# Performance work log

Measured on AMD Instinct MI355X. Metric: run time of the kernel, lower is better.

## Reference

```python
import jax, jax.numpy as jnp
import numpy as np

# Config mirrors cfg['cluster'] and point_cloud_range from init_kwargs
PCR = np.array([-51.2, -51.2, -5.0, 51.2, 51.2, 3.0], dtype=np.float32)
VOXEL_SIZE = 0.2
SIZE_X = 512  # floor((51.2 - (-51.2)) / 0.2)
EPS = 1.5
MIN_SAMPLES = 5
MIN_P_CLUSTER = 20


def _cluster(points):
    """Faithful jax version of Cluster.forward for batch_size == 1.

    voxel_down_sample -> DBSCAN (euclidean, eps, min_samples) on voxel coords
    -> drop clusters with < MIN_P_CLUSTER voxels -> scatter labels back to points.
    """
    N = points.shape[0]
    # --- voxel_down_sample ---
    coords = jnp.floor((points[:, 1:3] - PCR[:2]) / VOXEL_SIZE).astype(jnp.int32)  # (N,2) x,y
    merged = coords[:, 1] * SIZE_X + coords[:, 0]
    # static-size unique: padded entries get fill_value=-1 at the end
    uniq, inv = jnp.unique(merged, size=N, fill_value=-1, return_inverse=True)
    valid = uniq >= 0  # (N,) real voxels
    vox = jnp.stack([uniq % SIZE_X, uniq // SIZE_X], axis=1).astype(jnp.float32)  # (N,2)

    # --- DBSCAN on voxel coords ---
    d2 = jnp.sum((vox[:, None, :] - vox[None, :, :]) ** 2, axis=-1)  # (N,N)
    adj = (d2 <= EPS * EPS) & valid[:, None] & valid[None, :]  # includes self-edge
    core = (jnp.sum(adj, axis=1) >= MIN_SAMPLES) & valid  # sklearn counts self

    BIG = N  # sentinel > any label
    labels0 = jnp.where(core, jnp.arange(N), BIG)
    adj_core = adj & core[None, :]

    def min_core_neighbor(labels):
        return jnp.min(jnp.where(adj_core, labels[None, :], BIG), axis=1)

    def body(carry):
        labels, _ = carry
        new = jnp.where(core, jnp.minimum(labels, min_core_neighbor(labels)), labels)
        return new, jnp.any(new != labels)

    # min-label propagation = connected components over core-core eps graph
    labels, _ = jax.lax.while_loop(lambda c: c[1], body, (labels0, jnp.array(True)))

    # border points attach to a neighboring core cluster; otherwise noise (-1)
    nb = min_core_neighbor(labels)
    raw = jnp.where(core, labels, jnp.where(valid & (nb < BIG), nb, -1))  # root-id or -1

    # relabel root-ids to consecutive 0..k-1 (sklearn numbering by smallest core idx)
    roots = jnp.unique(raw, size=N, fill_value=BIG)  # sorted; BIG padding at end
    pos = jnp.searchsorted(roots, raw)
    dense = pos - (roots[0] == -1).astype(pos.dtype)
    dense = jnp.where(raw >= 0, dense, -1)

    # drop small clusters (by voxel count), keep remaining ids unchanged
    counts = jnp.zeros(N, jnp.int32).at[jnp.where(dense >= 0, dense, 0)].add(
        jnp.where(dense >= 0, 1, 0))
    keep = counts >= MIN_P_CLUSTER
    final = jnp.where((dense >= 0) & keep[jnp.clip(dense, 0, N - 1)], dense, -1)

    # scatter voxel labels back to points (points_inst_idx has points.dtype, like torch)
    pts_inst = final[inv].astype(points.dtype)
    max_num_inst = jnp.maximum(jnp.max(final) + 1, 0)
    return pts_inst, max_num_inst


def setup_inputs() -> dict:
    key = jax.random.key(0)
    N = 8192
    k1, k2, k3, k4, k5, k6, k7 = jax.random.split(key, 7)
    n_blobs = 64
    centers = jax.random.uniform(k1, (n_blobs, 2), minval=-48.0, maxval=48.0)
    assign = jax.random.randint(k2, (N,), 0, n_blobs)
    xy = centers[assign] + jax.random.normal(k3, (N, 2)) * 1.0
    noise = jax.random.uniform(k4, (N,)) < 0.2
    xy = jnp.where(noise[:, None], jax.random.uniform(k5, (N, 2), minval=-51.0, maxval=51.0), xy)
    xy = jnp.clip(xy, -51.0, 51.0)
    z = jax.random.uniform(k6, (N, 1), minval=-3.0, maxval=1.0)
    feat = jax.random.normal(k7, (N, 1))
    points = jnp.concatenate([jnp.zeros((N, 1)), xy, z, feat], axis=1).astype(jnp.float32)
    return {"points": points, "batch_size": 1}


def reference(points, batch_size):
    # voxel_down_sample asserts batch_size == 1; single-batch path.
    return _cluster(points)
```

## Files before the change

kernel.cpp:

```cpp
#include <hip/hip_runtime.h>
#include <stdint.h>


#define GRIDW 512
#define WPR 16
#define NWORDS 8192
#define NCELLS 262144
#define NONE 0xFFFFFFFFu

#define OFF_OCC    0
#define OFF_CNT    8192
#define OFF_ROOTBM 16384
#define OFF_KEEPBM 16640
#define OFF_CM     16896
#define OFF_LAB    25088
#define OFF_PRE    33280
#define OFF_RPRE   41472

__device__ __forceinline__ void hsum(uint32_t l, uint32_t c, uint32_t r,
                                     uint32_t& h0, uint32_t& h1) {
  uint32_t Wb = (c << 1) | (l >> 31);
  uint32_t Eb = (c >> 1) | (r << 31);
  h0 = Wb ^ c ^ Eb;
  h1 = (Wb & c) | (Eb & (Wb ^ c));
}

__device__ __forceinline__ uint32_t ge5(uint32_t a0, uint32_t a1, uint32_t b0,
                                        uint32_t b1, uint32_t c0, uint32_t c1) {
  uint32_t u0 = a0 ^ b0, cy = a0 & b0;
  uint32_t t = a1 ^ b1;
  uint32_t u1 = t ^ cy;
  uint32_t u2 = (a1 & b1) | (cy & t);
  uint32_t v0 = u0 ^ c0, k0 = u0 & c0;
  uint32_t t2 = u1 ^ c1;
  uint32_t v1 = t2 ^ k0;
  uint32_t k1 = (u1 & c1) | (k0 & t2);
  uint32_t v2 = u2 ^ k1;
  uint32_t v3 = u2 & k1;
  return v3 | (v2 & (v1 | v0));
}

__device__ __forceinline__ uint32_t aread(uint32_t* p) {
  return __hip_atomic_load(p, __ATOMIC_RELAXED, __HIP_MEMORY_SCOPE_AGENT);
}

__device__ __forceinline__ uint32_t findc(uint32_t* L, uint32_t x) {
  uint32_t r = x, p = aread(&L[r]);
  while (p != r) { r = p; p = aread(&L[r]); }
  while (x > r) {
    uint32_t nx = aread(&L[x]);
    if (nx <= r) break;
    atomicCAS(&L[x], nx, r);
    x = nx;
  }
  return r;
}

__device__ __forceinline__ void unite(uint32_t* L, uint32_t a, uint32_t b) {
  for (;;) {
    a = findc(L, a);
    b = findc(L, b);
    if (a == b) return;
    uint32_t lo = min(a, b), hi = max(a, b);
    if (atomicCAS(&L[hi], hi, lo) == hi) return;
    a = lo; b = hi;
  }
}

__global__ void k_vox(const float* __restrict__ pts, uint32_t* __restrict__ ws,
                      int npts) {
  int i = blockIdx.x * 256 + threadIdx.x;
  if (i >= npts) return;
  float x = pts[i * 5 + 1];
  float y = pts[i * 5 + 2];
  int cx = (int)floorf((x - (-51.2f)) / 0.2f);
  int cy = (int)floorf((y - (-51.2f)) / 0.2f);
  cx = min(max(cx, 0), GRIDW - 1);
  cy = min(max(cy, 0), GRIDW - 1);
  int cell = cy * GRIDW + cx;
  atomicOr(&ws[OFF_OCC + (cell >> 5)], 1u << (cell & 31));
}

__global__ void k_scan_cm(uint32_t* __restrict__ ws) {
  const uint32_t* occ = ws + OFF_OCC;
  int tid = threadIdx.x;
  if (blockIdx.x == 0) {
    __shared__ uint32_t wsum[4];
    ws[OFF_ROOTBM + tid] = 0u;
    ws[OFF_KEEPBM + tid] = 0u;
    int base = tid * 32;
    uint32_t s = 0;
    for (int j = 0; j < 32; j++) s += __popc(occ[base + j]);
    int lane = tid & 63, wv = tid >> 6;
    uint32_t inc = s;
    for (int d = 1; d < 64; d <<= 1) { uint32_t t = __shfl_up(inc, d); if (lane >= d) inc += t; }
    if (lane == 63) wsum[wv] = inc;
    __syncthreads();
    uint32_t woff = 0;
    for (int k = 0; k < wv; k++) woff += wsum[k];
    uint32_t excl = woff + inc - s;
    uint32_t* pre = ws + OFF_PRE;
    for (int j = 0; j < 32; j++) { pre[base + j] = excl; excl += __popc(occ[base + j]); }
  } else {
    int wi = (blockIdx.x - 1) * 256 + tid;
    ws[OFF_LAB + wi] = (uint32_t)wi;
    ws[OFF_CNT + wi] = 0u;
    uint32_t cB = occ[wi];
    int y = wi >> 4, wx = wi & 15;
    uint32_t lB = wx ? occ[wi - 1] : 0u;
    uint32_t rB = (wx < 15) ? occ[wi + 1] : 0u;
    uint32_t cA = 0, lA = 0, rA = 0, cC = 0, lC = 0, rC = 0;
    if (y > 0) { int wa = wi - WPR; cA = occ[wa]; lA = wx ? occ[wa - 1] : 0u; rA = (wx < 15) ? occ[wa + 1] : 0u; }
    if (y < GRIDW - 1) { int wc = wi + WPR; cC = occ[wc]; lC = wx ? occ[wc - 1] : 0u; rC = (wx < 15) ? occ[wc + 1] : 0u; }
    uint32_t a0, a1, b0, b1, c0, c1;
    hsum(lA, cA, rA, a0, a1); hsum(lB, cB, rB, b0, b1); hsum(lC, cC, rC, c0, c1);
    ws[OFF_CM + wi] = ge5(a0, a1, b0, b1, c0, c1) & cB;
  }
}

__global__ void k_merge(uint32_t* __restrict__ ws) {
  int cell = blockIdx.x * 256 + threadIdx.x;
  const uint32_t* occ = ws + OFF_OCC;
  const uint32_t* cm = ws + OFF_CM;
  const uint32_t* pre = ws + OFF_PRE;
  uint32_t* lab = ws + OFF_LAB;
  int wi = cell >> 5, b = cell & 31, wx = wi & 15;
  uint32_t cw = cm[wi];
  if (!((cw >> b) & 1)) return;
  int y = cell >> 9;
  uint32_t cB = occ[wi];
  int r = pre[wi] + __popc(cB & ((1u << b) - 1u));
  bool eC = (b < 31) ? ((cw >> (b + 1)) & 1) : ((wx < 15) ? (cm[wi + 1] & 1) : false);
  if (eC) unite(lab, r, (b < 31) ? r + 1 : pre[wi + 1]);
  if (y < GRIDW - 1) {
    uint32_t cmS = cm[wi + WPR];
    uint32_t occS = occ[wi + WPR];
    int rS = pre[wi + WPR];
    if ((cmS >> b) & 1) unite(lab, r, rS + __popc(occS & ((1u << b) - 1u)));
    bool seC = (b < 31) ? ((cmS >> (b + 1)) & 1) : ((wx < 15) ? (cm[wi + WPR + 1] & 1) : false);
    if (seC) unite(lab, r, (b < 31) ? rS + __popc(occS & ((2u << b) - 1u)) : pre[wi + WPR + 1]);
    bool swC = (b > 0) ? ((cmS >> (b - 1)) & 1) : ((wx > 0) ? (cm[wi + WPR - 1] >> 31) : false);
    if (swC) unite(lab, r, (b > 0) ? rS + __popc(occS & ((1u << (b - 1)) - 1u)) : rS - 1);
  }
}

__global__ void k_cb(uint32_t* __restrict__ ws) {
  int cell = blockIdx.x * 256 + threadIdx.x;
  int wi = cell >> 5, b = cell & 31, wx = wi & 15;
  const uint32_t* occ = ws + OFF_OCC;
  uint32_t cB = occ[wi];
  if (!((cB >> b) & 1)) return;
  const uint32_t* cm = ws + OFF_CM;
  const uint32_t* pre = ws + OFF_PRE;
  uint32_t* lab = ws + OFF_LAB;
  uint32_t* cnt = ws + OFF_CNT;
  int y = cell >> 9;
  uint32_t cw = cm[wi];
  int r = pre[wi] + __popc(cB & ((1u << b) - 1u));
  if ((cw >> b) & 1) {
    uint32_t root = findc(lab, r);
    lab[r] = root;
    if (root == (uint32_t)r) atomicOr(&ws[OFF_ROOTBM + (r >> 5)], 1u << (r & 31));
    atomicAdd(&cnt[root], 1u);
  } else {
    uint32_t m = NONE;
    bool wC = (b > 0) ? ((cw >> (b - 1)) & 1) : ((wx > 0) ? (cm[wi - 1] >> 31) : false);
    if (wC) m = min(m, findc(lab, (b > 0) ? r - 1 : (int)pre[wi] - 1));
    bool eC = (b < 31) ? ((cw >> (b + 1)) & 1) : ((wx < 15) ? (cm[wi + 1] & 1) : false);
    if (eC) m = min(m, findc(lab, (b < 31) ? r + 1 : pre[wi + 1]));
    if (y > 0) {
      uint32_t cmN = cm[wi - WPR], occN = occ[wi - WPR];
      int rN = pre[wi - WPR];
      if ((cmN >> b) & 1) m = min(m, findc(lab, rN + __popc(occN & ((1u << b) - 1u))));
      bool neC = (b < 31) ? ((cmN >> (b + 1)) & 1) : ((wx < 15) ? (cm[wi - WPR + 1] & 1) : false);
      if (neC) m = min(m, findc(lab, (b < 31) ? rN + __popc(occN & ((2u << b) - 1u)) : pre[wi - WPR + 1]));
      bool nwC = (b > 0) ? ((cmN >> (b - 1)) & 1) : ((wx > 0) ? (cm[wi - WPR - 1] >> 31) : false);
      if (nwC) m = min(m, findc(lab, (b > 0) ? rN + __popc(occN & ((1u << (b - 1)) - 1u)) : rN - 1));
    }
    if (y < GRIDW - 1) {
      uint32_t cmS = cm[wi + WPR], occS = occ[wi + WPR];
      int rS = pre[wi + WPR];
      if ((cmS >> b) & 1) m = min(m, findc(lab, rS + __popc(occS & ((1u << b) - 1u))));
      bool seC = (b < 31) ? ((cmS >> (b + 1)) & 1) : ((wx < 15) ? (cm[wi + WPR + 1] & 1) : false);
      if (seC) m = min(m, findc(lab, (b < 31) ? rS + __popc(occS & ((2u << b) - 1u)) : pre[wi + WPR + 1]));
      bool swC = (b > 0) ? ((cmS >> (b - 1)) & 1) : ((wx > 0) ? (cm[wi + WPR - 1] >> 31) : false);
      if (swC) m = min(m, findc(lab, (b > 0) ? rS + __popc(occS & ((1u << (b - 1)) - 1u)) : rS - 1));
    }
    lab[r] = m;
    if (m != NONE) atomicAdd(&cnt[m], 1u);
  }
}

__global__ void k_finish(uint32_t* __restrict__ ws, float* __restrict__ out,
                         int npts) {
  int tid = threadIdx.x;
  __shared__ uint32_t wsum[4];
  __shared__ int smax;
  if (tid == 0) smax = -1;
  __syncthreads();
  uint32_t rb = ws[OFF_ROOTBM + tid];
  uint32_t v = __popc(rb);
  int lane = tid & 63, wv = tid >> 6;
  uint32_t inc = v;
  for (int d = 1; d < 64; d <<= 1) { uint32_t t = __shfl_up(inc, d); if (lane >= d) inc += t; }
  if (lane == 63) wsum[wv] = inc;
  __syncthreads();
  uint32_t woff = 0;
  for (int k = 0; k < wv; k++) woff += wsum[k];
  uint32_t excl = woff + inc - v;
  ws[OFF_RPRE + tid] = excl;
  uint32_t keep = 0;
  int mx = -1, d = (int)excl;
  while (rb) {
    int b = __ffs(rb) - 1; rb &= rb - 1;
    int r = tid * 32 + b;
    if (ws[OFF_CNT + r] >= 20u) { keep |= 1u << b; mx = d; }
    d++;
  }
  ws[OFF_KEEPBM + tid] = keep;
  if (mx >= 0) atomicMax(&smax, mx);
  __syncthreads();
  if (tid == 0) out[npts] = (float)(smax + 1);
}

__global__ void k_scatter(const float* __restrict__ pts,
                          const uint32_t* __restrict__ ws,
                          float* __restrict__ out, int npts) {
  int i = blockIdx.x * 256 + threadIdx.x;
  if (i >= npts) return;
  float x = pts[i * 5 + 1];
  float y = pts[i * 5 + 2];
  int cx = (int)floorf((x - (-51.2f)) / 0.2f);
  int cy = (int)floorf((y - (-51.2f)) / 0.2f);
  cx = min(max(cx, 0), GRIDW - 1);
  cy = min(max(cy, 0), GRIDW - 1);
  int cell = cy * GRIDW + cx;
  int wi = cell >> 5;
  int r = ws[OFF_PRE + wi] + __popc(ws[OFF_OCC + wi] & ((1u << (cell & 31)) - 1u));
  uint32_t l = ws[OFF_LAB + r];
  float o = -1.0f;
  if (l != NONE && ((ws[OFF_KEEPBM + (l >> 5)] >> (l & 31)) & 1)) {
    int dnum = ws[OFF_RPRE + (l >> 5)] +
               __popc(ws[OFF_ROOTBM + (l >> 5)] & ((1u << (l & 31)) - 1u));
    o = (float)dnum;
  }
  out[i] = o;
}

extern "C" void kernel_launch(void* const* d_in, const int* in_sizes, int n_in,
                              void* d_out, int out_size, void* d_ws, size_t ws_size,
                              hipStream_t stream) {
  const float* pts = (const float*)d_in[0];
  int npts = in_sizes[0] / 5;
  uint32_t* ws = (uint32_t*)d_ws;
  float* out = (float*)d_out;
  int pblocks = (npts + 255) / 256;
  hipMemsetAsync(d_ws, 0, NWORDS * 4, stream);
  k_vox<<<pblocks, 256, 0, stream>>>(pts, ws, npts);
  k_scan_cm<<<33, 256, 0, stream>>>(ws);
  k_merge<<<NCELLS / 256, 256, 0, stream>>>(ws);
  k_cb<<<NCELLS / 256, 256, 0, stream>>>(ws);
  k_finish<<<1, 256, 0, stream>>>(ws, out, npts);
  k_scatter<<<pblocks, 256, 0, stream>>>(pts, ws, out, npts);
}
```

Measured before the change: 96.53 us.

## Fuse all clustering stages into one cooperative kernel with grid syncs

Replaces the memset and six separate kernel launches with a single cooperative kernel of 256 blocks. Stages are separated by grid-wide barriers, and grid-stride loops cover the cell and point work. This removes per-launch overhead and the inter-kernel gaps for a small workload. The cost is six grid syncs and lower parallelism in the per-cell stages, since 256 blocks now loop over 262144 cells.

```diff
diff --git a/kernel.cpp b/kernel.cpp
--- a/kernel.cpp
+++ b/kernel.cpp
@@ -1,5 +1,8 @@
 #include <hip/hip_runtime.h>
+#include <hip/hip_cooperative_groups.h>
 #include <stdint.h>
+
+namespace cg = cooperative_groups;
 
 
 #define GRIDW 512
@@ -67,27 +70,39 @@
   }
 }
 
-__global__ void k_vox(const float* __restrict__ pts, uint32_t* __restrict__ ws,
-                      int npts) {
-  int i = blockIdx.x * 256 + threadIdx.x;
-  if (i >= npts) return;
-  float x = pts[i * 5 + 1];
-  float y = pts[i * 5 + 2];
-  int cx = (int)floorf((x - (-51.2f)) / 0.2f);
-  int cy = (int)floorf((y - (-51.2f)) / 0.2f);
-  cx = min(max(cx, 0), GRIDW - 1);
-  cy = min(max(cy, 0), GRIDW - 1);
-  int cell = cy * GRIDW + cx;
-  atomicOr(&ws[OFF_OCC + (cell >> 5)], 1u << (cell & 31));
-}
-
-__global__ void k_scan_cm(uint32_t* __restrict__ ws) {
+__global__ __launch_bounds__(256) void k_all(const float* __restrict__ pts,
+                                             uint32_t* __restrict__ ws,
+                                             float* __restrict__ out,
+                                             int npts) {
+  cg::grid_group grid = cg::this_grid();
+  const int tid = threadIdx.x;
+  const int gtid = blockIdx.x * 256 + tid;
+  const int T = gridDim.x * 256;
+  __shared__ uint32_t wsum[4];
+  __shared__ int smax;
+
+  for (int i = gtid; i < NWORDS; i += T) {
+    ws[OFF_OCC + i] = 0u;
+    ws[OFF_CNT + i] = 0u;
+    ws[OFF_LAB + i] = (uint32_t)i;
+  }
+  if (gtid < 256) { ws[OFF_ROOTBM + gtid] = 0u; ws[OFF_KEEPBM + gtid] = 0u; }
+  grid.sync();
+
+  for (int i = gtid; i < npts; i += T) {
+    float x = pts[i * 5 + 1];
+    float y = pts[i * 5 + 2];
+    int cx = (int)floorf((x - (-51.2f)) / 0.2f);
+    int cy = (int)floorf((y - (-51.2f)) / 0.2f);
+    cx = min(max(cx, 0), GRIDW - 1);
+    cy = min(max(cy, 0), GRIDW - 1);
+    int cell = cy * GRIDW + cx;
+    atomicOr(&ws[OFF_OCC + (cell >> 5)], 1u << (cell & 31));
+  }
+  grid.sync();
+
   const uint32_t* occ = ws + OFF_OCC;
-  int tid = threadIdx.x;
   if (blockIdx.x == 0) {
-    __shared__ uint32_t wsum[4];
-    ws[OFF_ROOTBM + tid] = 0u;
-    ws[OFF_KEEPBM + tid] = 0u;
     int base = tid * 32;
     uint32_t s = 0;
     for (int j = 0; j < 32; j++) s += __popc(occ[base + j]);
@@ -102,149 +117,138 @@
     uint32_t* pre = ws + OFF_PRE;
     for (int j = 0; j < 32; j++) { pre[base + j] = excl; excl += __popc(occ[base + j]); }
   } else {
-    int wi = (blockIdx.x - 1) * 256 + tid;
-    ws[OFF_LAB + wi] = (uint32_t)wi;
-    ws[OFF_CNT + wi] = 0u;
-    uint32_t cB = occ[wi];
-    int y = wi >> 4, wx = wi & 15;
-    uint32_t lB = wx ? occ[wi - 1] : 0u;
-    uint32_t rB = (wx < 15) ? occ[wi + 1] : 0u;
-    uint32_t cA = 0, lA = 0, rA = 0, cC = 0, lC = 0, rC = 0;
-    if (y > 0) { int wa = wi - WPR; cA = occ[wa]; lA = wx ? occ[wa - 1] : 0u; rA = (wx < 15) ? occ[wa + 1] : 0u; }
-    if (y < GRIDW - 1) { int wc = wi + WPR; cC = occ[wc]; lC = wx ? occ[wc - 1] : 0u; rC = (wx < 15) ? occ[wc + 1] : 0u; }
-    uint32_t a0, a1, b0, b1, c0, c1;
-    hsum(lA, cA, rA, a0, a1); hsum(lB, cB, rB, b0, b1); hsum(lC, cC, rC, c0, c1);
-    ws[OFF_CM + wi] = ge5(a0, a1, b0, b1, c0, c1) & cB;
-  }
-}
-
-__global__ void k_merge(uint32_t* __restrict__ ws) {
-  int cell = blockIdx.x * 256 + threadIdx.x;
-  const uint32_t* occ = ws + OFF_OCC;
+    int wi = gtid - 256;
+    if (wi < NWORDS) {
+      uint32_t cB = occ[wi];
+      int y = wi >> 4, wx = wi & 15;
+      uint32_t lB = wx ? occ[wi - 1] : 0u;
+      uint32_t rB = (wx < 15) ? occ[wi + 1] : 0u;
+      uint32_t cA = 0, lA = 0, rA = 0, cC = 0, lC = 0, rC = 0;
+      if (y > 0) { int wa = wi - WPR; cA = occ[wa]; lA = wx ? occ[wa - 1] : 0u; rA = (wx < 15) ? occ[wa + 1] : 0u; }
+      if (y < GRIDW - 1) { int wc = wi + WPR; cC = occ[wc]; lC = wx ? occ[wc - 1] : 0u; rC = (wx < 15) ? occ[wc + 1] : 0u; }
+      uint32_t a0, a1, b0, b1, c0, c1;
+      hsum(lA, cA, rA, a0, a1); hsum(lB, cB, rB, b0, b1); hsum(lC, cC, rC, c0, c1);
+      ws[OFF_CM + wi] = ge5(a0, a1, b0, b1, c0, c1) & cB;
+    }
+  }
+  grid.sync();
+
   const uint32_t* cm = ws + OFF_CM;
   const uint32_t* pre = ws + OFF_PRE;
   uint32_t* lab = ws + OFF_LAB;
-  int wi = cell >> 5, b = cell & 31, wx = wi & 15;
-  uint32_t cw = cm[wi];
-  if (!((cw >> b) & 1)) return;
-  int y = cell >> 9;
-  uint32_t cB = occ[wi];
-  int r = pre[wi] + __popc(cB & ((1u << b) - 1u));
-  bool eC = (b < 31) ? ((cw >> (b + 1)) & 1) : ((wx < 15) ? (cm[wi + 1] & 1) : false);
-  if (eC) unite(lab, r, (b < 31) ? r + 1 : pre[wi + 1]);
-  if (y < GRIDW - 1) {
-    uint32_t cmS = cm[wi + WPR];
-    uint32_t occS = occ[wi + WPR];
-    int rS = pre[wi + WPR];
-    if ((cmS >> b) & 1) unite(lab, r, rS + __popc(occS & ((1u << b) - 1u)));
-    bool seC = (b < 31) ? ((cmS >> (b + 1)) & 1) : ((wx < 15) ? (cm[wi + WPR + 1] & 1) : false);
-    if (seC) unite(lab, r, (b < 31) ? rS + __popc(occS & ((2u << b) - 1u)) : pre[wi + WPR + 1]);
-    bool swC = (b > 0) ? ((cmS >> (b - 1)) & 1) : ((wx > 0) ? (cm[wi + WPR - 1] >> 31) : false);
-    if (swC) unite(lab, r, (b > 0) ? rS + __popc(occS & ((1u << (b - 1)) - 1u)) : rS - 1);
-  }
-}
-
-__global__ void k_cb(uint32_t* __restrict__ ws) {
-  int cell = blockIdx.x * 256 + threadIdx.x;
-  int wi = cell >> 5, b = cell & 31, wx = wi & 15;
-  const uint32_t* occ = ws + OFF_OCC;
-  uint32_t cB = occ[wi];
-  if (!((cB >> b) & 1)) return;
-  const uint32_t* cm = ws + OFF_CM;
-  const uint32_t* pre = ws + OFF_PRE;
-  uint32_t* lab = ws + OFF_LAB;
+  for (int cell = gtid; cell < NCELLS; cell += T) {
+    int wi = cell >> 5, b = cell & 31, wx = wi & 15;
+    uint32_t cw = cm[wi];
+    if (!((cw >> b) & 1)) continue;
+    int y = cell >> 9;
+    uint32_t cB = occ[wi];
+    int r = pre[wi] + __popc(cB & ((1u << b) - 1u));
+    bool eC = (b < 31) ? ((cw >> (b + 1)) & 1) : ((wx < 15) ? (cm[wi + 1] & 1) : false);
+    if (eC) unite(lab, r, (b < 31) ? r + 1 : pre[wi + 1]);
+    if (y < GRIDW - 1) {
+      uint32_t cmS = cm[wi + WPR];
+      uint32_t occS = occ[wi + WPR];
+      int rS = pre[wi + WPR];
+      if ((cmS >> b) & 1) unite(lab, r, rS + __popc(occS & ((1u << b) - 1u)));
+      bool seC = (b < 31) ? ((cmS >> (b + 1)) & 1) : ((wx < 15) ? (cm[wi + WPR + 1] & 1) : false);
+      if (seC) unite(lab, r, (b < 31) ? rS + __popc(occS & ((2u << b) - 1u)) : pre[wi + WPR + 1]);
+      bool swC = (b > 0) ? ((cmS >> (b - 1)) & 1) : ((wx > 0) ? (cm[wi + WPR - 1] >> 31) : false);
+      if (swC) unite(lab, r, (b > 0) ? rS + __popc(occS & ((1u << (b - 1)) - 1u)) : rS - 1);
+    }
+  }
+  grid.sync();
+
   uint32_t* cnt = ws + OFF_CNT;
-  int y = cell >> 9;
-  uint32_t cw = cm[wi];
-  int r = pre[wi] + __popc(cB & ((1u << b) - 1u));
-  if ((cw >> b) & 1) {
-    uint32_t root = findc(lab, r);
-    lab[r] = root;
-    if (root == (uint32_t)r) atomicOr(&ws[OFF_ROOTBM + (r >> 5)], 1u << (r & 31));
-    atomicAdd(&cnt[root], 1u);
-  } else {
-    uint32_t m = NONE;
-    bool wC = (b > 0) ? ((cw >> (b - 1)) & 1) : ((wx > 0) ? (cm[wi - 1] >> 31) : false);
-    if (wC) m = min(m, findc(lab, (b > 0) ? r - 1 : (int)pre[wi] - 1));
-    bool eC = (b < 31) ? ((cw >> (b + 1)) & 1) : ((wx < 15) ? (cm[wi + 1] & 1) : false);
-    if (eC) m = min(m, findc(lab, (b < 31) ? r + 1 : pre[wi + 1]));
-    if (y > 0) {
-      uint32_t cmN = cm[wi - WPR], occN = occ[wi - WPR];
-      int rN = pre[wi - WPR];
-      if ((cmN >> b) & 1) m = min(m, findc(lab, rN + __popc(occN & ((1u << b) - 1u))));
-      bool neC = (b < 31) ? ((cmN >> (b + 1)) & 1) : ((wx < 15) ? (cm[wi - WPR + 1] & 1) : false);
-      if (neC) m = min(m, findc(lab, (b < 31) ? rN + __popc(occN & ((2u << b) - 1u)) : pre[wi - WPR + 1]));
-      bool nwC = (b > 0) ? ((cmN >> (b - 1)) & 1) : ((wx > 0) ? (cm[wi - WPR - 1] >> 31) : false);
-      if (nwC) m = min(m, findc(lab, (b > 0) ? rN + __popc(occN & ((1u << (b - 1)) - 1u)) : rN - 1));
-    }
-    if (y < GRIDW - 1) {
-      uint32_t cmS = cm[wi + WPR], occS = occ[wi + WPR];
-      int rS = pre[wi + WPR];
-      if ((cmS >> b) & 1) m = min(m, findc(lab, rS + __popc(occS & ((1u << b) - 1u))));
-      bool seC = (b < 31) ? ((cmS >> (b + 1)) & 1) : ((wx < 15) ? (cm[wi + WPR + 1] & 1) : false);
-      if (seC) m = min(m, findc(lab, (b < 31) ? rS + __popc(occS & ((2u << b) - 1u)) : pre[wi + WPR + 1]));
-      bool swC = (b > 0) ? ((cmS >> (b - 1)) & 1) : ((wx > 0) ? (cm[wi + WPR - 1] >> 31) : false);
-      if (swC) m = min(m, findc(lab, (b > 0) ? rS + __popc(occS & ((1u << (b - 1)) - 1u)) : rS - 1));
-    }
-    lab[r] = m;
-    if (m != NONE) atomicAdd(&cnt[m], 1u);
-  }
-}
-
-__global__ void k_finish(uint32_t* __restrict__ ws, float* __restrict__ out,
-                         int npts) {
-  int tid = threadIdx.x;
-  __shared__ uint32_t wsum[4];
-  __shared__ int smax;
-  if (tid == 0) smax = -1;
-  __syncthreads();
-  uint32_t rb = ws[OFF_ROOTBM + tid];
-  uint32_t v = __popc(rb);
-  int lane = tid & 63, wv = tid >> 6;
-  uint32_t inc = v;
-  for (int d = 1; d < 64; d <<= 1) { uint32_t t = __shfl_up(inc, d); if (lane >= d) inc += t; }
-  if (lane == 63) wsum[wv] = inc;
-  __syncthreads();
-  uint32_t woff = 0;
-  for (int k = 0; k < wv; k++) woff += wsum[k];
-  uint32_t excl = woff + inc - v;
-  ws[OFF_RPRE + tid] = excl;
-  uint32_t keep = 0;
-  int mx = -1, d = (int)excl;
-  while (rb) {
-    int b = __ffs(rb) - 1; rb &= rb - 1;
-    int r = tid * 32 + b;
-    if (ws[OFF_CNT + r] >= 20u) { keep |= 1u << b; mx = d; }
-    d++;
-  }
-  ws[OFF_KEEPBM + tid] = keep;
-  if (mx >= 0) atomicMax(&smax, mx);
-  __syncthreads();
-  if (tid == 0) out[npts] = (float)(smax + 1);
-}
-
-__global__ void k_scatter(const float* __restrict__ pts,
-                          const uint32_t* __restrict__ ws,
-                          float* __restrict__ out, int npts) {
-  int i = blockIdx.x * 256 + threadIdx.x;
-  if (i >= npts) return;
-  float x = pts[i * 5 + 1];
-  float y = pts[i * 5 + 2];
-  int cx = (int)floorf((x - (-51.2f)) / 0.2f);
-  int cy = (int)floorf((y - (-51.2f)) / 0.2f);
-  cx = min(max(cx, 0), GRIDW - 1);
-  cy = min(max(cy, 0), GRIDW - 1);
-  int cell = cy * GRIDW + cx;
-  int wi = cell >> 5;
-  int r = ws[OFF_PRE + wi] + __popc(ws[OFF_OCC + wi] & ((1u << (cell & 31)) - 1u));
-  uint32_t l = ws[OFF_LAB + r];
-  float o = -1.0f;
-  if (l != NONE && ((ws[OFF_KEEPBM + (l >> 5)] >> (l & 31)) & 1)) {
-    int dnum = ws[OFF_RPRE + (l >> 5)] +
-               __popc(ws[OFF_ROOTBM + (l >> 5)] & ((1u << (l & 31)) - 1u));
-    o = (float)dnum;
-  }
-  out[i] = o;
+  for (int cell = gtid; cell < NCELLS; cell += T) {
+    int wi = cell >> 5, b = cell & 31, wx = wi & 15;
+    uint32_t cB = occ[wi];
+    if (!((cB >> b) & 1)) continue;
+    int y = cell >> 9;
+    uint32_t cw = cm[wi];
+    int r = pre[wi] + __popc(cB & ((1u << b) - 1u));
+    if ((cw >> b) & 1) {
+      uint32_t root = findc(lab, r);
+      lab[r] = root;
+      if (root == (uint32_t)r) atomicOr(&ws[OFF_ROOTBM + (r >> 5)], 1u << (r & 31));
+      atomicAdd(&cnt[root], 1u);
+    } else {
+      uint32_t m = NONE;
+      bool wC = (b > 0) ? ((cw >> (b - 1)) & 1) : ((wx > 0) ? (cm[wi - 1] >> 31) : false);
+      if (wC) m = min(m, findc(lab, (b > 0) ? r - 1 : (int)pre[wi] - 1));
+      bool eC = (b < 31) ? ((cw >> (b + 1)) & 1) : ((wx < 15) ? (cm[wi + 1] & 1) : false);
+      if (eC) m = min(m, findc(lab, (b < 31) ? r + 1 : pre[wi + 1]));
+      if (y > 0) {
+        uint32_t cmN = cm[wi - WPR], occN = occ[wi - WPR];
+        int rN = pre[wi - WPR];
+        if ((cmN >> b) & 1) m = min(m, findc(lab, rN + __popc(occN & ((1u << b) - 1u))));
+        bool neC = (b < 31) ? ((cmN >> (b + 1)) & 1) : ((wx < 15) ? (cm[wi - WPR + 1] & 1) : false);
+        if (neC) m = min(m, findc(lab, (b < 31) ? rN + __popc(occN & ((2u << b) - 1u)) : pre[wi - WPR + 1]));
+        bool nwC = (b > 0) ? ((cmN >> (b - 1)) & 1) : ((wx > 0) ? (cm[wi - WPR - 1] >> 31) : false);
+        if (nwC) m = min(m, findc(lab, (b > 0) ? rN + __popc(occN & ((1u << (b - 1)) - 1u)) : rN - 1));
+      }
+      if (y < GRIDW - 1) {
+        uint32_t cmS = cm[wi + WPR], occS = occ[wi + WPR];
+        int rS = pre[wi + WPR];
+        if ((cmS >> b) & 1) m = min(m, findc(lab, rS + __popc(occS & ((1u << b) - 1u))));
+        bool seC = (b < 31) ? ((cmS >> (b + 1)) & 1) : ((wx < 15) ? (cm[wi + WPR + 1] & 1) : false);
+        if (seC) m = min(m, findc(lab, (b < 31) ? rS + __popc(occS & ((2u << b) - 1u)) : pre[wi + WPR + 1]));
+        bool swC = (b > 0) ? ((cmS >> (b - 1)) & 1) : ((wx > 0) ? (cm[wi + WPR - 1] >> 31) : false);
+        if (swC) m = min(m, findc(lab, (b > 0) ? rS + __popc(occS & ((1u << (b - 1)) - 1u)) : rS - 1));
+      }
+      lab[r] = m;
+      if (m != NONE) atomicAdd(&cnt[m], 1u);
+    }
+  }
+  grid.sync();
+
+  if (blockIdx.x == 0) {
+    if (tid == 0) smax = -1;
+    __syncthreads();
+    uint32_t rb = ws[OFF_ROOTBM + tid];
+    uint32_t v = __popc(rb);
+    int lane = tid & 63, wv = tid >> 6;
+    uint32_t inc = v;
+    for (int d = 1; d < 64; d <<= 1) { uint32_t t = __shfl_up(inc, d); if (lane >= d) inc += t; }
+    if (lane == 63) wsum[wv] = inc;
+    __syncthreads();
+    uint32_t woff = 0;
+    for (int k = 0; k < wv; k++) woff += wsum[k];
+    uint32_t excl = woff + inc - v;
+    ws[OFF_RPRE + tid] = excl;
+    uint32_t keep = 0;
+    int mx = -1, d = (int)excl;
+    while (rb) {
+      int b = __ffs(rb) - 1; rb &= rb - 1;
+      int rr = tid * 32 + b;
+      if (ws[OFF_CNT + rr] >= 20u) { keep |= 1u << b; mx = d; }
+      d++;
+    }
+    ws[OFF_KEEPBM + tid] = keep;
+    if (mx >= 0) atomicMax(&smax, mx);
+    __syncthreads();
+    if (tid == 0) out[npts] = (float)(smax + 1);
+  }
+  grid.sync();
+
+  for (int i = gtid; i < npts; i += T) {
+    float x = pts[i * 5 + 1];
+    float y = pts[i * 5 + 2];
+    int cx = (int)floorf((x - (-51.2f)) / 0.2f);
+    int cy = (int)floorf((y - (-51.2f)) / 0.2f);
+    cx = min(max(cx, 0), GRIDW - 1);
+    cy = min(max(cy, 0), GRIDW - 1);
+    int cell = cy * GRIDW + cx;
+    int wi = cell >> 5;
+    int r = ws[OFF_PRE + wi] + __popc(ws[OFF_OCC + wi] & ((1u << (cell & 31)) - 1u));
+    uint32_t l = ws[OFF_LAB + r];
+    float o = -1.0f;
+    if (l != NONE && ((ws[OFF_KEEPBM + (l >> 5)] >> (l & 31)) & 1)) {
+      int dnum = ws[OFF_RPRE + (l >> 5)] +
+                 __popc(ws[OFF_ROOTBM + (l >> 5)] & ((1u << (l & 31)) - 1u));
+      o = (float)dnum;
+    }
+    out[i] = o;
+  }
 }
 
 extern "C" void kernel_launch(void* const* d_in, const int* in_sizes, int n_in,
@@ -254,12 +258,7 @@
   int npts = in_sizes[0] / 5;
   uint32_t* ws = (uint32_t*)d_ws;
   float* out = (float*)d_out;
-  int pblocks = (npts + 255) / 256;
-  hipMemsetAsync(d_ws, 0, NWORDS * 4, stream);
-  k_vox<<<pblocks, 256, 0, stream>>>(pts, ws, npts);
-  k_scan_cm<<<33, 256, 0, stream>>>(ws);
-  k_merge<<<NCELLS / 256, 256, 0, stream>>>(ws);
-  k_cb<<<NCELLS / 256, 256, 0, stream>>>(ws);
-  k_finish<<<1, 256, 0, stream>>>(ws, out, npts);
-  k_scatter<<<pblocks, 256, 0, stream>>>(pts, ws, out, npts);
-}
+  void* args[] = {(void*)&pts, (void*)&ws, (void*)&out, (void*)&npts};
+  hipLaunchCooperativeKernel(reinterpret_cast<void*>(k_all), dim3(256),
+                             dim3(256), args, 0, stream);
+}
```

Measured after the change: 253.3 us. +162.5%, slower.
